# Kernel tuning notes

Measured on AMD Instinct MI355X. Metric: run time of the kernel, lower is better.

The kernel has to match this reference:

```python
import jax, jax.numpy as jnp
import numpy as np

N, IC, H, OC, E = 50000, 128, 128, 64, 800000
EPS = 1e-5


def _sage(x, src, dst, wl, wr, b):
    # PyG SAGEConv (mean aggr): out = lin_l(mean_j x_j) + lin_r(x)
    msg = x[src]                                    # [E, d] gather
    s = jax.ops.segment_sum(msg, dst, num_segments=N)
    cnt = jax.ops.segment_sum(jnp.ones((src.shape[0],), x.dtype), dst, num_segments=N)
    mean = s / jnp.clip(cnt, 1.0)[:, None]
    return mean @ wl.T + b + x @ wr.T


def _bn_relu(x, g, be):
    # training-mode BatchNorm1d over node axis (biased var), then ReLU
    m = jnp.mean(x, axis=0)
    v = jnp.mean((x - m) ** 2, axis=0)
    return jax.nn.relu((x - m) * jax.lax.rsqrt(v + EPS) * g + be)


def setup_inputs() -> dict:
    key = jax.random.key(0)
    ks = jax.random.split(key, 16)
    d = {
        "x": jax.random.normal(ks[0], (N, IC), jnp.float32),
        "ei": jax.random.randint(ks[1], (2, E), 0, N, jnp.int32),
        # SAGEConv 1..3: lin_l (with bias) on aggregated, lin_r (no bias) on root
        "w1l": jax.random.normal(ks[2], (H, IC), jnp.float32) / np.sqrt(IC),
        "w1r": jax.random.normal(ks[3], (H, IC), jnp.float32) / np.sqrt(IC),
        "b1c": jnp.zeros((H,), jnp.float32),
        "w2l": jax.random.normal(ks[4], (H, H), jnp.float32) / np.sqrt(H),
        "w2r": jax.random.normal(ks[5], (H, H), jnp.float32) / np.sqrt(H),
        "b2c": jnp.zeros((H,), jnp.float32),
        "w3l": jax.random.normal(ks[6], (H, H), jnp.float32) / np.sqrt(H),
        "w3r": jax.random.normal(ks[7], (H, H), jnp.float32) / np.sqrt(H),
        "b3c": jnp.zeros((H,), jnp.float32),
        # BatchNorm affine params
        "g1": jnp.ones((H,), jnp.float32), "be1": jnp.zeros((H,), jnp.float32),
        "g2": jnp.ones((H,), jnp.float32), "be2": jnp.zeros((H,), jnp.float32),
        "g3": jnp.ones((H,), jnp.float32), "be3": jnp.zeros((H,), jnp.float32),
        # head Linear
        "wh": jax.random.normal(ks[8], (OC, H), jnp.float32) / np.sqrt(H),
        "bh": jnp.zeros((OC,), jnp.float32),
    }
    return d


def reference(x, ei, w1l, w1r, b1c, w2l, w2r, b2c, w3l, w3r, b3c,
              g1, be1, g2, be2, g3, be3, wh, bh):
    src, dst = ei[0], ei[1]
    h = _bn_relu(_sage(x, src, dst, w1l, w1r, b1c), g1, be1)
    # dropout omitted (deterministic reference / eval semantics)
    h = _bn_relu(_sage(h, src, dst, w2l, w2r, b2c), g2, be2)
    h = _bn_relu(_sage(h, src, dst, w3l, w3r, b3c), g3, be3)
    return h @ wh.T + bh
```

## Files before the change

kernel.cpp:

```cpp
#include <hip/hip_runtime.h>

static constexpr int FC = 128;

typedef __attribute__((ext_vector_type(8))) __bf16 bf16x8;
typedef __attribute__((ext_vector_type(4))) float f32x4;

__device__ __forceinline__ unsigned short f2bf(float f) {
  unsigned u = __float_as_uint(f);
  unsigned r = (u + 0x7FFF + ((u >> 16) & 1)) >> 16;
  return (unsigned short)r;
}
__device__ __forceinline__ float bf2f(unsigned short h) {
  return __uint_as_float((unsigned)h << 16);
}

__global__ __launch_bounds__(256) void zero_kernel(int* __restrict__ deg,
                                                   float* __restrict__ stats, int n) {
  int i = blockIdx.x * 256 + threadIdx.x;
  if (i < n) deg[i] = 0;
  if (i < 768) stats[i] = 0.f;
}

__global__ __launch_bounds__(256) void convert_kernel(
    const float* __restrict__ x, const float* __restrict__ w1l, const float* __restrict__ w1r,
    const float* __restrict__ w2l, const float* __restrict__ w2r,
    const float* __restrict__ w3l, const float* __restrict__ w3r,
    const float* __restrict__ wh,
    unsigned short* __restrict__ x_bf, unsigned short* __restrict__ wc1,
    unsigned short* __restrict__ wc2, unsigned short* __restrict__ wc3,
    unsigned short* __restrict__ whb, int nx8, int nxb) {
  int b = blockIdx.x;
  int t = threadIdx.x;
  if (b < nxb) {
    int i = b * 256 + t;
    if (i >= nx8) return;
    const float* p = x + (size_t)i * 8;
    float4 a = *reinterpret_cast<const float4*>(p);
    float4 c = *reinterpret_cast<const float4*>(p + 4);
    ushort4 o0 = {f2bf(a.x), f2bf(a.y), f2bf(a.z), f2bf(a.w)};
    ushort4 o1 = {f2bf(c.x), f2bf(c.y), f2bf(c.z), f2bf(c.w)};
    unsigned short* q = x_bf + (size_t)i * 8;
    *reinterpret_cast<ushort4*>(q) = o0;
    *reinterpret_cast<ushort4*>(q + 4) = o1;
    return;
  }
  int r = b - nxb;
  if (r < 48) {
    int layer = r >> 4;
    const float* wl = layer == 0 ? w1l : (layer == 1 ? w2l : w3l);
    const float* wr = layer == 0 ? w1r : (layer == 1 ? w2r : w3r);
    unsigned short* out = layer == 0 ? wc1 : (layer == 1 ? wc2 : wc3);
    int i = (r & 15) * 256 + t;
    int row = i >> 5;
    int k8 = (i & 31) * 8;
    const float* src = (k8 < 128) ? (wl + (size_t)row * 128 + k8)
                                  : (wr + (size_t)row * 128 + (k8 - 128));
    float4 a = *reinterpret_cast<const float4*>(src);
    float4 c = *reinterpret_cast<const float4*>(src + 4);
    ushort4 o0 = {f2bf(a.x), f2bf(a.y), f2bf(a.z), f2bf(a.w)};
    ushort4 o1 = {f2bf(c.x), f2bf(c.y), f2bf(c.z), f2bf(c.w)};
    unsigned short* q = out + (size_t)row * 256 + k8;
    *reinterpret_cast<ushort4*>(q) = o0;
    *reinterpret_cast<ushort4*>(q + 4) = o1;
  } else {
    int i = (r - 48) * 256 + t;
    const float* p = wh + (size_t)i * 8;
    float4 a = *reinterpret_cast<const float4*>(p);
    float4 c = *reinterpret_cast<const float4*>(p + 4);
    ushort4 o0 = {f2bf(a.x), f2bf(a.y), f2bf(a.z), f2bf(a.w)};
    ushort4 o1 = {f2bf(c.x), f2bf(c.y), f2bf(c.z), f2bf(c.w)};
    unsigned short* q = whb + (size_t)i * 8;
    *reinterpret_cast<ushort4*>(q) = o0;
    *reinterpret_cast<ushort4*>(q + 4) = o1;
  }
}

__global__ void count_kernel(const int* __restrict__ dst, int* __restrict__ deg,
                             int* __restrict__ rank, int e) {
  int i = blockIdx.x * blockDim.x + threadIdx.x;
  if (i < e) rank[i] = atomicAdd(&deg[dst[i]], 1);
}

__global__ __launch_bounds__(256) void scan1_kernel(const int* __restrict__ deg,
                                                    int* __restrict__ bsum, int n) {
  int i = blockIdx.x * 256 + threadIdx.x;
  int v = (i < n) ? deg[i] : 0;
  __shared__ int ls[256];
  ls[threadIdx.x] = v;
  __syncthreads();
  for (int d = 128; d > 0; d >>= 1) {
    if (threadIdx.x < (unsigned)d) ls[threadIdx.x] += ls[threadIdx.x + d];
    __syncthreads();
  }
  if (threadIdx.x == 0) bsum[blockIdx.x] = ls[0];
}

__global__ __launch_bounds__(256) void scan23_kernel(const int* __restrict__ deg,
                                                     const int* __restrict__ bsum,
                                                     int* __restrict__ off, int n, int nb) {
  __shared__ int bls[256];
  __shared__ int ls[256];
  int t = threadIdx.x;
  int bv = (t < nb) ? bsum[t] : 0;
  bls[t] = bv;
  __syncthreads();
  for (int d = 1; d < 256; d <<= 1) {
    int u = (t >= d) ? bls[t - d] : 0;
    __syncthreads();
    bls[t] += u;
    __syncthreads();
  }
  int i = blockIdx.x * 256 + t;
  int v = (i < n) ? deg[i] : 0;
  ls[t] = v;
  __syncthreads();
  for (int d = 1; d < 256; d <<= 1) {
    int u = (t >= d) ? ls[t - d] : 0;
    __syncthreads();
    ls[t] += u;
    __syncthreads();
  }
  int base = blockIdx.x ? bls[blockIdx.x - 1] : 0;
  if (i < n) off[i] = base + ls[t] - v;
  if (blockIdx.x == 0 && t == 0) off[n] = bls[nb - 1];
}

__global__ void fill_kernel(const int* __restrict__ src, const int* __restrict__ dst,
                            const int* __restrict__ rank, const int* __restrict__ off,
                            int* __restrict__ csr, int e) {
  int i = blockIdx.x * blockDim.x + threadIdx.x;
  if (i < e) csr[off[dst[i]] + rank[i]] = src[i];
}

template <bool BNIN>
__global__ __launch_bounds__(256) void aggregate_kernel(const unsigned short* __restrict__ x,
                                                        const int* __restrict__ off,
                                                        const int* __restrict__ csr,
                                                        unsigned short* __restrict__ agg,
                                                        const float* __restrict__ stats,
                                                        const float* __restrict__ g,
                                                        const float* __restrict__ be,
                                                        float invn, int n) {
  int hw = (int)((blockIdx.x * blockDim.x + threadIdx.x) >> 5);
  int lane = threadIdx.x & 31;
  if (hw >= n) return;

  float sc0 = 1.f, sc1 = 1.f, sc2 = 1.f, sc3 = 1.f;
  float sh0 = 0.f, sh1 = 0.f, sh2 = 0.f, sh3 = 0.f;
  if (BNIN) {
    int c0 = lane * 4;
    float4 s  = *reinterpret_cast<const float4*>(stats + c0);
    float4 s2 = *reinterpret_cast<const float4*>(stats + 128 + c0);
    float4 gv = *reinterpret_cast<const float4*>(g + c0);
    float4 bv = *reinterpret_cast<const float4*>(be + c0);
    float m0 = s.x * invn, m1 = s.y * invn, m2 = s.z * invn, m3 = s.w * invn;
    sc0 = gv.x * rsqrtf(fmaxf(s2.x * invn - m0 * m0, 0.f) + 1e-5f);
    sc1 = gv.y * rsqrtf(fmaxf(s2.y * invn - m1 * m1, 0.f) + 1e-5f);
    sc2 = gv.z * rsqrtf(fmaxf(s2.z * invn - m2 * m2, 0.f) + 1e-5f);
    sc3 = gv.w * rsqrtf(fmaxf(s2.w * invn - m3 * m3, 0.f) + 1e-5f);
    sh0 = bv.x - m0 * sc0; sh1 = bv.y - m1 * sc1;
    sh2 = bv.z - m2 * sc2; sh3 = bv.w - m3 * sc3;
  }

  int s0 = off[hw], s1 = off[hw + 1];
  float a0 = 0.f, a1 = 0.f, a2 = 0.f, a3 = 0.f;

#define ACCV(v)                                                                   \
  {                                                                               \
    float t0 = bf2f((v).x), t1 = bf2f((v).y), t2 = bf2f((v).z), t3 = bf2f((v).w); \
    if (BNIN) {                                                                   \
      t0 = fmaxf(fmaf(t0, sc0, sh0), 0.f);                                        \
      t1 = fmaxf(fmaf(t1, sc1, sh1), 0.f);                                        \
      t2 = fmaxf(fmaf(t2, sc2, sh2), 0.f);                                        \
      t3 = fmaxf(fmaf(t3, sc3, sh3), 0.f);                                        \
    }                                                                             \
    a0 += t0; a1 += t1; a2 += t2; a3 += t3;                                       \
  }

  int j = s0;
  for (; j + 8 <= s1; j += 8) {
    int i0 = csr[j],     i1 = csr[j + 1], i2 = csr[j + 2], i3 = csr[j + 3];
    int i4 = csr[j + 4], i5 = csr[j + 5], i6 = csr[j + 6], i7 = csr[j + 7];
    ushort4 v0 = *reinterpret_cast<const ushort4*>(x + (size_t)i0 * FC + lane * 4);
    ushort4 v1 = *reinterpret_cast<const ushort4*>(x + (size_t)i1 * FC + lane * 4);
    ushort4 v2 = *reinterpret_cast<const ushort4*>(x + (size_t)i2 * FC + lane * 4);
    ushort4 v3 = *reinterpret_cast<const ushort4*>(x + (size_t)i3 * FC + lane * 4);
    ushort4 v4 = *reinterpret_cast<const ushort4*>(x + (size_t)i4 * FC + lane * 4);
    ushort4 v5 = *reinterpret_cast<const ushort4*>(x + (size_t)i5 * FC + lane * 4);
    ushort4 v6 = *reinterpret_cast<const ushort4*>(x + (size_t)i6 * FC + lane * 4);
    ushort4 v7 = *reinterpret_cast<const ushort4*>(x + (size_t)i7 * FC + lane * 4);
    ACCV(v0) ACCV(v1) ACCV(v2) ACCV(v3) ACCV(v4) ACCV(v5) ACCV(v6) ACCV(v7)
  }
  if (j + 4 <= s1) {
    int i0 = csr[j], i1 = csr[j + 1], i2 = csr[j + 2], i3 = csr[j + 3];
    ushort4 v0 = *reinterpret_cast<const ushort4*>(x + (size_t)i0 * FC + lane * 4);
    ushort4 v1 = *reinterpret_cast<const ushort4*>(x + (size_t)i1 * FC + lane * 4);
    ushort4 v2 = *reinterpret_cast<const ushort4*>(x + (size_t)i2 * FC + lane * 4);
    ushort4 v3 = *reinterpret_cast<const ushort4*>(x + (size_t)i3 * FC + lane * 4);
    ACCV(v0) ACCV(v1) ACCV(v2) ACCV(v3)
    j += 4;
  }
  for (; j < s1; j++) {
    int i0 = csr[j];
    ushort4 v0 = *reinterpret_cast<const ushort4*>(x + (size_t)i0 * FC + lane * 4);
    ACCV(v0)
  }
#undef ACCV

  int d = s1 - s0;
  float inv = 1.0f / (float)(d > 0 ? d : 1);
  ushort4 o = {f2bf(a0 * inv), f2bf(a1 * inv), f2bf(a2 * inv), f2bf(a3 * inv)};
  *reinterpret_cast<ushort4*>(agg + (size_t)hw * FC + lane * 4) = o;
}

template <int NCOLS, int KTOT, bool DUAL, bool OUT_BF, bool STATS, bool BNIN>
__global__ __launch_bounds__(256) void gemm_kernel(const unsigned short* __restrict__ A1,
                                                   const unsigned short* __restrict__ A2,
                                                   const unsigned short* __restrict__ W,
                                                   const float* __restrict__ bias,
                                                   void* __restrict__ Cout,
                                                   float* __restrict__ statsOut,
                                                   const float* __restrict__ statsIn,
                                                   const float* __restrict__ g,
                                                   const float* __restrict__ be,
                                                   float invn, int nrows) {
  constexpr int NKT = KTOT / 32;
  constexpr int NCF = NCOLS / 16;
  constexpr int RB = KTOT * 2;
  constexpr int WBYTES = NCOLS * KTOT * 2;
  __shared__ __align__(16) unsigned char Wl[WBYTES];
  __shared__ float scv[128], shv[128];

  int t = threadIdx.x;

  {
    constexpr int CH = WBYTES / 16 / 256;
#pragma unroll
    for (int c = 0; c < CH; c++) {
      int byte = (c * 256 + t) * 16;
      int row = byte / RB;
      int cb = byte % RB;
      float4 v = *reinterpret_cast<const float4*>(reinterpret_cast<const char*>(W) + byte);
      *reinterpret_cast<float4*>(Wl + row * RB + (cb ^ ((row & 7) << 4))) = v;
    }
  }

  if (BNIN && t < 128) {
    float mean = statsIn[t] * invn;
    float var = fmaxf(statsIn[128 + t] * invn - mean * mean, 0.f);
    float s = g[t] * rsqrtf(var + 1e-5f);
    scv[t] = s;
    shv[t] = be[t] - mean * s;
  }

  int w = t >> 6;
  int l = t & 63;
  int lm = l & 15;
  int hi = l >> 4;
  int lk = hi * 8;
  int row = blockIdx.x * 64 + w * 16 + lm;
  int rclamp = min(row, nrows - 1);

  bf16x8 a[NKT];
#pragma unroll
  for (int kt = 0; kt < NKT; kt++) {
    const unsigned short* Ap;
    int kk;
    if (!DUAL || kt < NKT / 2) { Ap = A1; kk = kt * 32; }
    else                       { Ap = A2; kk = (kt - NKT / 2) * 32; }
    a[kt] = *reinterpret_cast<const bf16x8*>(Ap + (size_t)rclamp * 128 + kk + lk);
  }

  f32x4 acc[NCF];
#pragma unroll
  for (int cf = 0; cf < NCF; cf++) acc[cf] = {0.f, 0.f, 0.f, 0.f};

  __syncthreads();

  if (BNIN) {
#pragma unroll
    for (int kt = 0; kt < NKT; kt++) {
      if (!DUAL || kt >= NKT / 2) {
        int ch0 = (DUAL ? (kt - NKT / 2) : kt) * 32 + lk;
#pragma unroll
        for (int j = 0; j < 8; j++) {
          float v = (float)a[kt][j];
          v = fmaxf(fmaf(v, scv[ch0 + j], shv[ch0 + j]), 0.f);
          a[kt][j] = (__bf16)v;
        }
      }
    }
  }

#pragma unroll
  for (int kt = 0; kt < NKT; kt++) {
#pragma unroll
    for (int cf = 0; cf < NCF; cf++) {
      int r = cf * 16 + lm;
      int cb = kt * 64 + hi * 16;
      bf16x8 b = *reinterpret_cast<const bf16x8*>(Wl + r * RB + (cb ^ ((r & 7) << 4)));
      acc[cf] = __builtin_amdgcn_mfma_f32_16x16x32_bf16(a[kt], b, acc[cf], 0, 0, 0);
    }
  }

  __shared__ float wsum[4][NCOLS];
  __shared__ float wsq[4][NCOLS];

  int orow0 = blockIdx.x * 64 + w * 16 + hi * 4;
#pragma unroll
  for (int cf = 0; cf < NCF; cf++) {
    int col = cf * 16 + lm;
    float bs = bias[col];
    float s = 0.f, s2 = 0.f;
#pragma unroll
    for (int r = 0; r < 4; r++) {
      int orow = orow0 + r;
      bool ok = orow < nrows;
      float v = acc[cf][r] + bs;
      if (ok) {
        if (OUT_BF)
          ((unsigned short*)Cout)[(size_t)orow * NCOLS + col] = f2bf(v);
        else
          ((float*)Cout)[(size_t)orow * NCOLS + col] = v;
      }
      if (STATS) {
        float vv = ok ? v : 0.f;
        s += vv; s2 += vv * vv;
      }
    }
    if (STATS) {
      s  += __shfl_xor(s, 16);  s  += __shfl_xor(s, 32);
      s2 += __shfl_xor(s2, 16); s2 += __shfl_xor(s2, 32);
      if (l < 16) { wsum[w][col] = s; wsq[w][col] = s2; }
    }
  }
  if (STATS) {
    __syncthreads();
    if (t < NCOLS) {
      atomicAdd(&statsOut[t], wsum[0][t] + wsum[1][t] + wsum[2][t] + wsum[3][t]);
    } else if (t < 2 * NCOLS) {
      int c = t - NCOLS;
      atomicAdd(&statsOut[t], wsq[0][c] + wsq[1][c] + wsq[2][c] + wsq[3][c]);
    }
  }
}

extern "C" void kernel_launch(void* const* d_in, const int* in_sizes, int n_in,
                              void* d_out, int out_size, void* d_ws, size_t ws_size,
                              hipStream_t stream) {
  const float* x   = (const float*)d_in[0];
  const int*   ei  = (const int*)d_in[1];
  const float* w1l = (const float*)d_in[2];
  const float* w1r = (const float*)d_in[3];
  const float* b1c = (const float*)d_in[4];
  const float* w2l = (const float*)d_in[5];
  const float* w2r = (const float*)d_in[6];
  const float* b2c = (const float*)d_in[7];
  const float* w3l = (const float*)d_in[8];
  const float* w3r = (const float*)d_in[9];
  const float* b3c = (const float*)d_in[10];
  const float* g1  = (const float*)d_in[11];
  const float* be1 = (const float*)d_in[12];
  const float* g2  = (const float*)d_in[13];
  const float* be2 = (const float*)d_in[14];
  const float* g3  = (const float*)d_in[15];
  const float* be3 = (const float*)d_in[16];
  const float* wh  = (const float*)d_in[17];
  const float* bh  = (const float*)d_in[18];

  int n = in_sizes[0] / FC;
  int e = in_sizes[1] / 2;
  const int* srcI = ei;
  const int* dstI = ei + e;

  char* p = (char*)d_ws;
  auto take = [&](size_t bytes) {
    char* q = p;
    p += (bytes + 255) & ~(size_t)255;
    return q;
  };
  int nb = (n + 255) / 256;
  int* deg  = (int*)take((size_t)n * 4);
  int* off  = (int*)take((size_t)(n + 1) * 4);
  int* bsum = (int*)take((size_t)nb * 4);
  int* rank = (int*)take((size_t)e * 4);
  int* csr  = (int*)take((size_t)e * 4);
  unsigned short* x_bf = (unsigned short*)take((size_t)n * FC * 2);
  unsigned short* agg  = (unsigned short*)take((size_t)n * FC * 2);
  unsigned short* h1   = (unsigned short*)take((size_t)n * FC * 2);
  unsigned short* h2   = (unsigned short*)take((size_t)n * FC * 2);
  unsigned short* wc1  = (unsigned short*)take(128 * 256 * 2);
  unsigned short* wc2  = (unsigned short*)take(128 * 256 * 2);
  unsigned short* wc3  = (unsigned short*)take(128 * 256 * 2);
  unsigned short* whb  = (unsigned short*)take(64 * 128 * 2);
  float* stats = (float*)take(3 * 256 * 4);

  float invn = 1.0f / (float)n;
  int nx8 = n * 16;
  int nxb = (nx8 + 255) / 256;

  zero_kernel<<<nb, 256, 0, stream>>>(deg, stats, n);
  convert_kernel<<<nxb + 52, 256, 0, stream>>>(x, w1l, w1r, w2l, w2r, w3l, w3r, wh,
                                               x_bf, wc1, wc2, wc3, whb, nx8, nxb);

  count_kernel<<<(e + 255) / 256, 256, 0, stream>>>(dstI, deg, rank, e);
  scan1_kernel<<<nb, 256, 0, stream>>>(deg, bsum, n);
  scan23_kernel<<<nb, 256, 0, stream>>>(deg, bsum, off, n, nb);
  fill_kernel<<<(e + 255) / 256, 256, 0, stream>>>(srcI, dstI, rank, off, csr, e);

  int gb = (n + 63) / 64;
  int ab = (n + 7) / 8;

  aggregate_kernel<false><<<ab, 256, 0, stream>>>(x_bf, off, csr, agg, nullptr, nullptr,
                                                  nullptr, invn, n);
  gemm_kernel<128, 256, true, true, true, false><<<gb, 256, 0, stream>>>(
      agg, x_bf, wc1, b1c, h1, stats, nullptr, nullptr, nullptr, invn, n);

  aggregate_kernel<true><<<ab, 256, 0, stream>>>(h1, off, csr, agg, stats, g1, be1, invn, n);
  gemm_kernel<128, 256, true, true, true, true><<<gb, 256, 0, stream>>>(
      agg, h1, wc2, b2c, h2, stats + 256, stats, g1, be1, invn, n);

  aggregate_kernel<true><<<ab, 256, 0, stream>>>(h2, off, csr, agg, stats + 256, g2, be2, invn, n);
  gemm_kernel<128, 256, true, true, true, true><<<gb, 256, 0, stream>>>(
      agg, h2, wc3, b3c, h1, stats + 512, stats + 256, g2, be2, invn, n);

  gemm_kernel<64, 128, false, false, false, true><<<gb, 256, 0, stream>>>(
      h1, nullptr, whb, bh, d_out, nullptr, stats + 512, g3, be3, invn, n);
}
```

Before: 275.6 us.

## Quantize gathered node features to per-row int8 for neighbor aggregation

Every aggregation pass now gathers neighbor rows from an int8 copy with one fp32 scale per row, instead of from the bf16 feature rows. The convert kernel and the first two GEMMs write this quantized copy, taking a row-wise absolute max via lane shuffles. The goal is to halve the bytes moved by the random-access gather, which dominates the aggregate kernels. In exchange, each edge now needs an extra scattered scale load, the GEMM epilogue does extra work, and int8 rounding error may loosen accuracy against the reference.

```diff
diff --git a/kernel.cpp b/kernel.cpp
--- a/kernel.cpp
+++ b/kernel.cpp
@@ -12,6 +12,10 @@
 }
 __device__ __forceinline__ float bf2f(unsigned short h) {
   return __uint_as_float((unsigned)h << 16);
+}
+__device__ __forceinline__ unsigned pk_i8x4(int q0, int q1, int q2, int q3) {
+  return (unsigned)(q0 & 0xff) | ((unsigned)(q1 & 0xff) << 8) |
+         ((unsigned)(q2 & 0xff) << 16) | ((unsigned)(q3 & 0xff) << 24);
 }
 
 __global__ __launch_bounds__(256) void zero_kernel(int* __restrict__ deg,
@@ -26,25 +30,34 @@
     const float* __restrict__ w2l, const float* __restrict__ w2r,
     const float* __restrict__ w3l, const float* __restrict__ w3r,
     const float* __restrict__ wh,
-    unsigned short* __restrict__ x_bf, unsigned short* __restrict__ wc1,
+    unsigned short* __restrict__ x_bf, unsigned* __restrict__ xi8,
+    float* __restrict__ xsc,
+    unsigned short* __restrict__ wc1,
     unsigned short* __restrict__ wc2, unsigned short* __restrict__ wc3,
-    unsigned short* __restrict__ whb, int nx8, int nxb) {
+    unsigned short* __restrict__ whb, int n, int nxq) {
   int b = blockIdx.x;
   int t = threadIdx.x;
-  if (b < nxb) {
-    int i = b * 256 + t;
-    if (i >= nx8) return;
-    const float* p = x + (size_t)i * 8;
-    float4 a = *reinterpret_cast<const float4*>(p);
-    float4 c = *reinterpret_cast<const float4*>(p + 4);
-    ushort4 o0 = {f2bf(a.x), f2bf(a.y), f2bf(a.z), f2bf(a.w)};
-    ushort4 o1 = {f2bf(c.x), f2bf(c.y), f2bf(c.z), f2bf(c.w)};
-    unsigned short* q = x_bf + (size_t)i * 8;
-    *reinterpret_cast<ushort4*>(q) = o0;
-    *reinterpret_cast<ushort4*>(q + 4) = o1;
+  if (b < nxq) {
+    int row = b * 8 + (t >> 5);
+    int lane = t & 31;
+    if (row >= n) return;
+    float4 a = *reinterpret_cast<const float4*>(x + (size_t)row * FC + lane * 4);
+    ushort4 o = {f2bf(a.x), f2bf(a.y), f2bf(a.z), f2bf(a.w)};
+    *reinterpret_cast<ushort4*>(x_bf + (size_t)row * FC + lane * 4) = o;
+    float m = fmaxf(fmaxf(fabsf(a.x), fabsf(a.y)), fmaxf(fabsf(a.z), fabsf(a.w)));
+    m = fmaxf(m, __shfl_xor(m, 1));
+    m = fmaxf(m, __shfl_xor(m, 2));
+    m = fmaxf(m, __shfl_xor(m, 4));
+    m = fmaxf(m, __shfl_xor(m, 8));
+    m = fmaxf(m, __shfl_xor(m, 16));
+    float inv = 127.0f / fmaxf(m, 1e-30f);
+    int q0 = (int)rintf(a.x * inv), q1 = (int)rintf(a.y * inv);
+    int q2 = (int)rintf(a.z * inv), q3 = (int)rintf(a.w * inv);
+    xi8[(size_t)row * 32 + lane] = pk_i8x4(q0, q1, q2, q3);
+    if (lane == 0) xsc[row] = m * (1.0f / 127.0f);
     return;
   }
-  int r = b - nxb;
+  int r = b - nxq;
   if (r < 48) {
     int layer = r >> 4;
     const float* wl = layer == 0 ? w1l : (layer == 1 ? w2l : w3l);
@@ -133,7 +146,8 @@
 }
 
 template <bool BNIN>
-__global__ __launch_bounds__(256) void aggregate_kernel(const unsigned short* __restrict__ x,
+__global__ __launch_bounds__(256) void aggregate_kernel(const unsigned* __restrict__ xi8,
+                                                        const float* __restrict__ xsc,
                                                         const int* __restrict__ off,
                                                         const int* __restrict__ csr,
                                                         unsigned short* __restrict__ agg,
@@ -165,45 +179,47 @@
   int s0 = off[hw], s1 = off[hw + 1];
   float a0 = 0.f, a1 = 0.f, a2 = 0.f, a3 = 0.f;
 
-#define ACCV(v)                                                                   \
-  {                                                                               \
-    float t0 = bf2f((v).x), t1 = bf2f((v).y), t2 = bf2f((v).z), t3 = bf2f((v).w); \
-    if (BNIN) {                                                                   \
-      t0 = fmaxf(fmaf(t0, sc0, sh0), 0.f);                                        \
-      t1 = fmaxf(fmaf(t1, sc1, sh1), 0.f);                                        \
-      t2 = fmaxf(fmaf(t2, sc2, sh2), 0.f);                                        \
-      t3 = fmaxf(fmaf(t3, sc3, sh3), 0.f);                                        \
-    }                                                                             \
-    a0 += t0; a1 += t1; a2 += t2; a3 += t3;                                       \
+#define ACCV(u, sv)                                               \
+  {                                                               \
+    float q0 = (float)(((int)(u) << 24) >> 24);                   \
+    float q1 = (float)(((int)(u) << 16) >> 24);                   \
+    float q2 = (float)(((int)(u) << 8) >> 24);                    \
+    float q3 = (float)((int)(u) >> 24);                           \
+    if (BNIN) {                                                   \
+      a0 += fmaxf(fmaf(q0, (sv) * sc0, sh0), 0.f);                \
+      a1 += fmaxf(fmaf(q1, (sv) * sc1, sh1), 0.f);                \
+      a2 += fmaxf(fmaf(q2, (sv) * sc2, sh2), 0.f);                \
+      a3 += fmaxf(fmaf(q3, (sv) * sc3, sh3), 0.f);                \
+    } else {                                                      \
+      a0 = fmaf(q0, (sv), a0);                                    \
+      a1 = fmaf(q1, (sv), a1);                                    \
+      a2 = fmaf(q2, (sv), a2);                                    \
+      a3 = fmaf(q3, (sv), a3);                                    \
+    }                                                             \
   }
 
   int j = s0;
   for (; j + 8 <= s1; j += 8) {
     int i0 = csr[j],     i1 = csr[j + 1], i2 = csr[j + 2], i3 = csr[j + 3];
     int i4 = csr[j + 4], i5 = csr[j + 5], i6 = csr[j + 6], i7 = csr[j + 7];
-    ushort4 v0 = *reinterpret_cast<const ushort4*>(x + (size_t)i0 * FC + lane * 4);
-    ushort4 v1 = *reinterpret_cast<const ushort4*>(x + (size_t)i1 * FC + lane * 4);
-    ushort4 v2 = *reinterpret_cast<const ushort4*>(x + (size_t)i2 * FC + lane * 4);
-    ushort4 v3 = *reinterpret_cast<const ushort4*>(x + (size_t)i3 * FC + lane * 4);
-    ushort4 v4 = *reinterpret_cast<const ushort4*>(x + (size_t)i4 * FC + lane * 4);
-    ushort4 v5 = *reinterpret_cast<const ushort4*>(x + (size_t)i5 * FC + lane * 4);
-    ushort4 v6 = *reinterpret_cast<const ushort4*>(x + (size_t)i6 * FC + lane * 4);
-    ushort4 v7 = *reinterpret_cast<const ushort4*>(x + (size_t)i7 * FC + lane * 4);
-    ACCV(v0) ACCV(v1) ACCV(v2) ACCV(v3) ACCV(v4) ACCV(v5) ACCV(v6) ACCV(v7)
-  }
-  if (j + 4 <= s1) {
-    int i0 = csr[j], i1 = csr[j + 1], i2 = csr[j + 2], i3 = csr[j + 3];
-    ushort4 v0 = *reinterpret_cast<const ushort4*>(x + (size_t)i0 * FC + lane * 4);
-    ushort4 v1 = *reinterpret_cast<const ushort4*>(x + (size_t)i1 * FC + lane * 4);
-    ushort4 v2 = *reinterpret_cast<const ushort4*>(x + (size_t)i2 * FC + lane * 4);
-    ushort4 v3 = *reinterpret_cast<const ushort4*>(x + (size_t)i3 * FC + lane * 4);
-    ACCV(v0) ACCV(v1) ACCV(v2) ACCV(v3)
-    j += 4;
+    unsigned u0 = xi8[(size_t)i0 * 32 + lane];
+    unsigned u1 = xi8[(size_t)i1 * 32 + lane];
+    unsigned u2 = xi8[(size_t)i2 * 32 + lane];
+    unsigned u3 = xi8[(size_t)i3 * 32 + lane];
+    unsigned u4 = xi8[(size_t)i4 * 32 + lane];
+    unsigned u5 = xi8[(size_t)i5 * 32 + lane];
+    unsigned u6 = xi8[(size_t)i6 * 32 + lane];
+    unsigned u7 = xi8[(size_t)i7 * 32 + lane];
+    float sv0 = xsc[i0], sv1 = xsc[i1], sv2 = xsc[i2], sv3 = xsc[i3];
+    float sv4 = xsc[i4], sv5 = xsc[i5], sv6 = xsc[i6], sv7 = xsc[i7];
+    ACCV(u0, sv0) ACCV(u1, sv1) ACCV(u2, sv2) ACCV(u3, sv3)
+    ACCV(u4, sv4) ACCV(u5, sv5) ACCV(u6, sv6) ACCV(u7, sv7)
   }
   for (; j < s1; j++) {
     int i0 = csr[j];
-    ushort4 v0 = *reinterpret_cast<const ushort4*>(x + (size_t)i0 * FC + lane * 4);
-    ACCV(v0)
+    unsigned u0 = xi8[(size_t)i0 * 32 + lane];
+    float sv0 = xsc[i0];
+    ACCV(u0, sv0)
   }
 #undef ACCV
 
@@ -213,12 +229,14 @@
   *reinterpret_cast<ushort4*>(agg + (size_t)hw * FC + lane * 4) = o;
 }
 
-template <int NCOLS, int KTOT, bool DUAL, bool OUT_BF, bool STATS, bool BNIN>
+template <int NCOLS, int KTOT, bool DUAL, bool OUT_BF, bool STATS, bool BNIN, bool OUT_I8>
 __global__ __launch_bounds__(256) void gemm_kernel(const unsigned short* __restrict__ A1,
                                                    const unsigned short* __restrict__ A2,
                                                    const unsigned short* __restrict__ W,
                                                    const float* __restrict__ bias,
                                                    void* __restrict__ Cout,
+                                                   unsigned char* __restrict__ h8,
+                                                   float* __restrict__ hsc,
                                                    float* __restrict__ statsOut,
                                                    const float* __restrict__ statsIn,
                                                    const float* __restrict__ g,
@@ -303,6 +321,29 @@
     }
   }
 
+#pragma unroll
+  for (int cf = 0; cf < NCF; cf++) {
+    float bs = bias[cf * 16 + lm];
+#pragma unroll
+    for (int r = 0; r < 4; r++) acc[cf][r] += bs;
+  }
+
+  float qinv[4], qs[4];
+  if (OUT_I8) {
+#pragma unroll
+    for (int r = 0; r < 4; r++) {
+      float m = 0.f;
+#pragma unroll
+      for (int cf = 0; cf < NCF; cf++) m = fmaxf(m, fabsf(acc[cf][r]));
+      m = fmaxf(m, __shfl_xor(m, 1));
+      m = fmaxf(m, __shfl_xor(m, 2));
+      m = fmaxf(m, __shfl_xor(m, 4));
+      m = fmaxf(m, __shfl_xor(m, 8));
+      qinv[r] = 127.0f / fmaxf(m, 1e-30f);
+      qs[r] = m * (1.0f / 127.0f);
+    }
+  }
+
   __shared__ float wsum[4][NCOLS];
   __shared__ float wsq[4][NCOLS];
 
@@ -310,18 +351,19 @@
 #pragma unroll
   for (int cf = 0; cf < NCF; cf++) {
     int col = cf * 16 + lm;
-    float bs = bias[col];
     float s = 0.f, s2 = 0.f;
 #pragma unroll
     for (int r = 0; r < 4; r++) {
       int orow = orow0 + r;
       bool ok = orow < nrows;
-      float v = acc[cf][r] + bs;
+      float v = acc[cf][r];
       if (ok) {
         if (OUT_BF)
           ((unsigned short*)Cout)[(size_t)orow * NCOLS + col] = f2bf(v);
         else
           ((float*)Cout)[(size_t)orow * NCOLS + col] = v;
+        if (OUT_I8)
+          h8[(size_t)orow * NCOLS + col] = (unsigned char)((int)rintf(v * qinv[r]) & 0xff);
       }
       if (STATS) {
         float vv = ok ? v : 0.f;
@@ -332,6 +374,13 @@
       s  += __shfl_xor(s, 16);  s  += __shfl_xor(s, 32);
       s2 += __shfl_xor(s2, 16); s2 += __shfl_xor(s2, 32);
       if (l < 16) { wsum[w][col] = s; wsq[w][col] = s2; }
+    }
+  }
+  if (OUT_I8 && lm == 0) {
+#pragma unroll
+    for (int r = 0; r < 4; r++) {
+      int orow = orow0 + r;
+      if (orow < nrows) hsc[orow] = qs[r];
     }
   }
   if (STATS) {
@@ -389,6 +438,8 @@
   unsigned short* agg  = (unsigned short*)take((size_t)n * FC * 2);
   unsigned short* h1   = (unsigned short*)take((size_t)n * FC * 2);
   unsigned short* h2   = (unsigned short*)take((size_t)n * FC * 2);
+  unsigned char*  ai8  = (unsigned char*)take((size_t)n * FC);
+  float*          asc  = (float*)take((size_t)n * 4);
   unsigned short* wc1  = (unsigned short*)take(128 * 256 * 2);
   unsigned short* wc2  = (unsigned short*)take(128 * 256 * 2);
   unsigned short* wc3  = (unsigned short*)take(128 * 256 * 2);
@@ -396,12 +447,12 @@
   float* stats = (float*)take(3 * 256 * 4);
 
   float invn = 1.0f / (float)n;
-  int nx8 = n * 16;
-  int nxb = (nx8 + 255) / 256;
+  int nxq = (n + 7) / 8;
 
   zero_kernel<<<nb, 256, 0, stream>>>(deg, stats, n);
-  convert_kernel<<<nxb + 52, 256, 0, stream>>>(x, w1l, w1r, w2l, w2r, w3l, w3r, wh,
-                                               x_bf, wc1, wc2, wc3, whb, nx8, nxb);
+  convert_kernel<<<nxq + 52, 256, 0, stream>>>(x, w1l, w1r, w2l, w2r, w3l, w3r, wh,
+                                               x_bf, (unsigned*)ai8, asc,
+                                               wc1, wc2, wc3, whb, n, nxq);
 
   count_kernel<<<(e + 255) / 256, 256, 0, stream>>>(dstI, deg, rank, e);
   scan1_kernel<<<nb, 256, 0, stream>>>(deg, bsum, n);
@@ -411,19 +462,21 @@
   int gb = (n + 63) / 64;
   int ab = (n + 7) / 8;
 
-  aggregate_kernel<false><<<ab, 256, 0, stream>>>(x_bf, off, csr, agg, nullptr, nullptr,
-                                                  nullptr, invn, n);
-  gemm_kernel<128, 256, true, true, true, false><<<gb, 256, 0, stream>>>(
-      agg, x_bf, wc1, b1c, h1, stats, nullptr, nullptr, nullptr, invn, n);
-
-  aggregate_kernel<true><<<ab, 256, 0, stream>>>(h1, off, csr, agg, stats, g1, be1, invn, n);
-  gemm_kernel<128, 256, true, true, true, true><<<gb, 256, 0, stream>>>(
-      agg, h1, wc2, b2c, h2, stats + 256, stats, g1, be1, invn, n);
-
-  aggregate_kernel<true><<<ab, 256, 0, stream>>>(h2, off, csr, agg, stats + 256, g2, be2, invn, n);
-  gemm_kernel<128, 256, true, true, true, true><<<gb, 256, 0, stream>>>(
-      agg, h2, wc3, b3c, h1, stats + 512, stats + 256, g2, be2, invn, n);
-
-  gemm_kernel<64, 128, false, false, false, true><<<gb, 256, 0, stream>>>(
-      h1, nullptr, whb, bh, d_out, nullptr, stats + 512, g3, be3, invn, n);
-}
+  aggregate_kernel<false><<<ab, 256, 0, stream>>>((const unsigned*)ai8, asc, off, csr, agg,
+                                                  nullptr, nullptr, nullptr, invn, n);
+  gemm_kernel<128, 256, true, true, true, false, true><<<gb, 256, 0, stream>>>(
+      agg, x_bf, wc1, b1c, h1, ai8, asc, stats, nullptr, nullptr, nullptr, invn, n);
+
+  aggregate_kernel<true><<<ab, 256, 0, stream>>>((const unsigned*)ai8, asc, off, csr, agg,
+                                                 stats, g1, be1, invn, n);
+  gemm_kernel<128, 256, true, true, true, true, true><<<gb, 256, 0, stream>>>(
+      agg, h1, wc2, b2c, h2, ai8, asc, stats + 256, stats, g1, be1, invn, n);
+
+  aggregate_kernel<true><<<ab, 256, 0, stream>>>((const unsigned*)ai8, asc, off, csr, agg,
+                                                 stats + 256, g2, be2, invn, n);
+  gemm_kernel<128, 256, true, true, true, true, false><<<gb, 256, 0, stream>>>(
+      agg, h2, wc3, b3c, h1, nullptr, nullptr, stats + 512, stats + 256, g2, be2, invn, n);
+
+  gemm_kernel<64, 128, false, false, false, true, false><<<gb, 256, 0, stream>>>(
+      h1, nullptr, whb, bh, d_out, nullptr, nullptr, nullptr, stats + 512, g3, be3, invn, n);
+}
```

Measured after the change: 261.7 us. -5.1%, faster.
